# Performance work log

Measured on AMD Instinct MI355X. Metric: run time of the kernel, lower is better.

## Reference

```python
import jax, jax.numpy as jnp
import numpy as np
from jax.scipy.special import gammaln

T_STEPS, N_GRID, NMUL = 730, 10000, 2
NEARZERO = 1e-5
LENF = 15  # unit-hydrograph length used by UH_gamma routing
STAT_NAMES = ["parFC", "parK0", "parK1", "parK2", "parLP", "parPERC", "parUZL",
              "parTT", "parCFMAX", "parCFR", "parCWH", "parC", "parRT", "parAC"]
BOUNDS = {"parBETA": (1.0, 6.0), "parFC": (50.0, 1000.0), "parK0": (0.05, 0.9),
          "parK1": (0.01, 0.5), "parK2": (0.001, 0.2), "parLP": (0.2, 1.0),
          "parPERC": (0.0, 10.0), "parUZL": (0.0, 100.0), "parTT": (-2.5, 2.5),
          "parCFMAX": (0.5, 10.0), "parCFR": (0.0, 0.1), "parCWH": (0.0, 0.2),
          "parBETAET": (0.3, 5.0), "parC": (0.0, 1.0), "parRT": (0.0, 20.0),
          "parAC": (0.0, 2500.0)}
ROUT_A = (0.0, 2.9)
ROUT_B = (0.0, 6.5)


def _scale(p, lo, hi):
    # change_param_range: affine map of [0,1]-normalized params to physical bounds
    return p * (hi - lo) + lo


def setup_inputs() -> dict:
    key = jax.random.key(0)
    ks = jax.random.split(key, 7)
    prcp = jax.random.uniform(ks[0], (T_STEPS, N_GRID)) * 10.0          # mm/day
    tmean = jax.random.uniform(ks[1], (T_STEPS, N_GRID)) * 30.0 - 10.0  # deg C, spans parTT range
    pet = jax.random.uniform(ks[2], (T_STEPS, N_GRID)) * 5.0            # mm/day
    x_phy = jnp.stack([prcp, tmean, pet], axis=-1).astype(jnp.float32)
    ac_all = jax.random.uniform(ks[3], (N_GRID,)) * 2500.0              # drainage area per unit basin
    elev_all = jax.random.uniform(ks[4], (N_GRID,)) * 3000.0            # elevation
    params_dy = jax.random.uniform(ks[5], (T_STEPS, N_GRID, 2 * NMUL))  # dynamic: parBETA, parBETAET
    params_stat = jax.random.uniform(ks[6], (N_GRID, 14 * NMUL + 2))    # 14 static phy + 2 routing
    return {"x_phy": x_phy, "ac_all": ac_all, "elev_all": elev_all,
            "params_dy": params_dy, "params_stat": params_stat}


def _forward(x_phy, ac_all, elev_all, params_dy, params_stat):
    T, G, _ = x_phy.shape
    P, Tair, PET = x_phy[..., 0], x_phy[..., 1], x_phy[..., 2]
    # expand forcing to nmul parameter components
    Pm = jnp.broadcast_to(P[..., None], (T, G, NMUL))
    Tm = jnp.broadcast_to(Tair[..., None], (T, G, NMUL))
    PETm = jnp.broadcast_to(PET[..., None], (T, G, NMUL))
    Ac = jnp.broadcast_to(ac_all[:, None], (G, NMUL))

    # dynamic (per-timestep) params; dy_drop=0.0 -> bernoulli drop mask is all zeros,
    # so the dynamic values are used directly at every step
    dy = params_dy.reshape(T, G, 2, NMUL)
    parBETA = _scale(dy[:, :, 0], *BOUNDS["parBETA"])
    parBETAET = _scale(dy[:, :, 1], *BOUNDS["parBETAET"])

    # static params: [G, 14, NMUL]
    stat = params_stat[:, :14 * NMUL].reshape(G, 14, NMUL)
    sp = {n: _scale(stat[:, i], *BOUNDS[n]) for i, n in enumerate(STAT_NAMES)}
    rout_a = _scale(params_stat[:, 14 * NMUL], *ROUT_A)
    rout_b = _scale(params_stat[:, 14 * NMUL + 1], *ROUT_B)

    def step(carry, xt):
        SNOWPACK, MELTWATER, SM, SUZ, SLZ = carry
        Pt, Tt, PETt, beta, betaet = xt
        rain_mask = (Tt >= sp["parTT"]).astype(Pt.dtype)
        RAIN = Pt * rain_mask
        SNOW = Pt * (1.0 - rain_mask)
        # --- snow bucket ---
        SNOWPACK = SNOWPACK + SNOW
        melt = jnp.maximum(sp["parCFMAX"] * (Tt - sp["parTT"]), 0.0)
        melt = jnp.minimum(melt, SNOWPACK)
        MELTWATER = MELTWATER + melt
        SNOWPACK = SNOWPACK - melt
        refreeze = jnp.maximum(sp["parCFR"] * sp["parCFMAX"] * (sp["parTT"] - Tt), 0.0)
        refreeze = jnp.minimum(refreeze, MELTWATER)
        SNOWPACK = SNOWPACK + refreeze
        MELTWATER = MELTWATER - refreeze
        tosoil = jnp.maximum(MELTWATER - sp["parCWH"] * SNOWPACK, 0.0)
        MELTWATER = MELTWATER - tosoil
        # --- soil bucket ---
        soil_wetness = jnp.clip((SM / sp["parFC"]) ** beta, 0.0, 1.0)
        recharge = (RAIN + tosoil) * soil_wetness
        SM = SM + RAIN + tosoil - recharge
        excess = jnp.maximum(SM - sp["parFC"], 0.0)
        SM = SM - excess
        evapfactor = jnp.clip(SM / (sp["parLP"] * sp["parFC"]), 0.0, 1.0) ** betaet
        ETact = jnp.minimum(SM, PETt * evapfactor)
        SM = jnp.maximum(SM - ETact, NEARZERO)
        # capillary rise from lower groundwater zone (parC)
        capillary = jnp.minimum(SLZ, sp["parC"] * SLZ * (1.0 - jnp.minimum(SM / sp["parFC"], 1.0)))
        SM = jnp.maximum(SM + capillary, NEARZERO)
        SLZ = jnp.maximum(SLZ - capillary, NEARZERO)
        # --- groundwater buckets ---
        SUZ = SUZ + recharge + excess
        PERC = jnp.minimum(SUZ, sp["parPERC"])
        SUZ = SUZ - PERC
        Q0 = sp["parK0"] * jnp.maximum(SUZ - sp["parUZL"], 0.0)
        SUZ = SUZ - Q0
        Q1 = sp["parK1"] * SUZ
        SUZ = SUZ - Q1
        SLZ = SLZ + PERC
        # HBV 2.0 regional groundwater loss (area-dependent via parRT / parAC; reconstructed)
        gw_loss = jnp.minimum(SLZ, sp["parRT"] * jnp.clip(1.0 - Ac / (sp["parAC"] + NEARZERO), 0.0, 1.0))
        SLZ = SLZ - gw_loss
        Q2 = sp["parK2"] * SLZ
        SLZ = SLZ - Q2
        Qt = Q0 + Q1 + Q2
        return (SNOWPACK, MELTWATER, SM, SUZ, SLZ), Qt

    init = tuple(jnp.full((G, NMUL), 1e-3, dtype=x_phy.dtype) for _ in range(5))
    _, Qsimmu = jax.lax.scan(step, init, (Pm, Tm, PETm, parBETA, parBETAET))
    Qsim = Qsimmu.mean(-1)  # [T, G]; muwts=None -> uniform average over nmul components

    # --- gamma unit-hydrograph routing (UH_gamma + causal UH_conv) ---
    a = jnp.maximum(rout_a, 0.0) + 0.1       # [G]
    theta = jnp.maximum(rout_b, 0.0) + 0.5   # [G]
    t = jnp.arange(LENF, dtype=Qsim.dtype) + 0.5  # [LENF]
    w = (jnp.exp(-gammaln(a))[None, :] * theta[None, :] ** (-a[None, :])
         * t[:, None] ** (a[None, :] - 1.0) * jnp.exp(-t[:, None] / theta[None, :]))
    w = w / w.sum(0)  # [LENF, G], normalized UH weights
    # causal grouped conv: flow[t] = sum_k w[k] * Qsim[t-k]
    Qpad = jnp.pad(Qsim, ((LENF - 1, 0), (0, 0)))
    flow = jnp.zeros_like(Qsim)
    for k in range(LENF):  # fixed, small tap count
        flow = flow + w[k][None, :] * Qpad[LENF - 1 - k: LENF - 1 - k + T]
    return flow[..., None]  # [T, G, 1] routed streamflow


def reference(x_phy, ac_all, elev_all, params_dy, params_stat):
    return _forward(x_phy, ac_all, elev_all, params_dy, params_stat)
```

## Files before the change

### kernel.cpp

```cpp
#include <hip/hip_runtime.h>


#define TS 730
#define NG 10000
#define CH 15
#define NCHUNK 49
#define XSTRIDE (NG * 3)
#define DSTRIDE (NG * 4)

#define AS1 __attribute__((address_space(1)))
#define AS3 __attribute__((address_space(3)))
#define WAIT_VMCNT(n) __builtin_amdgcn_s_waitcnt(((n) & 15) | 0x70 | 0xF00 | (((n) >> 4) << 14))
#define WAIT_LGKM0    __builtin_amdgcn_s_waitcnt(0xC07F)

__device__ __forceinline__ void gload16(const float* g, float* l) {
    __builtin_amdgcn_global_load_lds((const AS1 void*)g, (AS3 void*)l, 16, 0, 0);
}
__device__ __forceinline__ float powpos(float x, float b) {
    return __builtin_amdgcn_exp2f(b * __builtin_amdgcn_logf(x));
}
__device__ __forceinline__ float med3(float x, float lo, float hi) {
    return __builtin_amdgcn_fmed3f(x, lo, hi);
}

__global__ __launch_bounds__(64, 1) void hbv_fused(
    const float* __restrict__ x_phy,
    const float* __restrict__ ac_all,
    const float* __restrict__ params_dy,
    const float* __restrict__ params_stat,
    float* __restrict__ out)
{
    __shared__ float xls0[1536], xls1[1536];
    __shared__ float dls0[2048], dls1[2048];

    const int lane = threadIdx.x & 63;
    const int m    = lane >> 5;
    const int cell = lane & 31;
    const int g0   = blockIdx.x * 32;
    const int g    = g0 + cell;
    const int gl   = g < NG ? g : NG - 1;
    const int g0r  = (g0 <= NG - 32) ? g0 : NG - 32;
    const int co   = cell + (g0 - g0r);
    const int cl   = co < 31 ? co : 31;

    const float* ps = params_stat + (size_t)gl * 30;
    const float FC    = ps[0  + m] * 950.f   + 50.f;
    const float K0    = ps[2  + m] * 0.85f   + 0.05f;
    const float K1    = ps[4  + m] * 0.49f   + 0.01f;
    const float K2    = ps[6  + m] * 0.199f  + 0.001f;
    const float LP    = ps[8  + m] * 0.8f    + 0.2f;
    const float PERCp = ps[10 + m] * 10.f;
    const float UZL   = ps[12 + m] * 100.f;
    const float TTp   = ps[14 + m] * 5.f     - 2.5f;
    const float CFMAX = ps[16 + m] * 9.5f    + 0.5f;
    const float CFR   = ps[18 + m] * 0.1f;
    const float CWH   = ps[20 + m] * 0.2f;
    const float Cc    = ps[22 + m];
    const float RT    = ps[24 + m] * 20.f;
    const float ACp   = ps[26 + m] * 2500.f;
    const float ra    = ps[28] * 2.9f;
    const float rb    = ps[29] * 6.5f;

    const float Acv     = ac_all[gl];
    const float invFC   = 1.f / FC;
    const float invLPFC = 1.f / (LP * FC);
    const float CFRC    = CFR * CFMAX;
    const float gwcap   = RT * fminf(fmaxf(1.f - Acv / (ACp + 1e-5f), 0.f), 1.f);

    const float a     = fmaxf(ra, 0.f) + 0.1f;
    const float th    = fmaxf(rb, 0.f) + 0.5f;
    const float am1   = a - 1.f;
    const float nl2e  = 1.44269504f / th;
    float w[CH];
    float wsum = 0.f;
#pragma unroll
    for (int k = 0; k < CH; ++k) {
        const float tk = (float)k + 0.5f;
        const float v  = __builtin_amdgcn_exp2f(am1 * __builtin_amdgcn_logf(tk) - tk * nl2e);
        w[k] = v; wsum += v;
    }
    const float wn = 0.5f / wsum;
#pragma unroll
    for (int k = 0; k < CH; ++k) w[k] *= wn;

    int offx[6], offd[8];
#pragma unroll
    for (int i = 0; i < 6; ++i) {
        int idx = i * 64 + lane;
        idx = idx < 360 ? idx : 359;
        const int row = idx / 24;
        const int col = idx - row * 24;
        offx[i] = row * XSTRIDE + col * 4;
    }
#pragma unroll
    for (int i = 0; i < 8; ++i) {
        int idx = i * 64 + lane;
        idx = idx < 480 ? idx : 479;
        const int row = idx >> 5;
        const int col = idx & 31;
        offd[i] = row * DSTRIDE + col * 4;
    }
    const float* xbase = x_phy     + (size_t)g0r * 3;
    const float* dbase = params_dy + (size_t)g0r * 4;

    auto issue = [&](int cc, float* xl, float* dl) {
        if (cc == NCHUNK - 1) {
#pragma unroll
            for (int i = 0; i < 6; ++i) {
                int idx = i * 64 + lane; idx = idx < 360 ? idx : 359;
                const int row = idx / 24, col = idx - row * 24;
                int t = cc * CH + row; t = t < TS ? t : TS - 1;
                gload16(xbase + (size_t)t * XSTRIDE + col * 4, xl + i * 256);
            }
#pragma unroll
            for (int i = 0; i < 8; ++i) {
                int idx = i * 64 + lane; idx = idx < 480 ? idx : 479;
                const int row = idx >> 5, col = idx & 31;
                int t = cc * CH + row; t = t < TS ? t : TS - 1;
                gload16(dbase + (size_t)t * DSTRIDE + col * 4, dl + i * 256);
            }
        } else {
            const float* xp = xbase + (size_t)cc * CH * XSTRIDE;
            const float* dp = dbase + (size_t)cc * CH * DSTRIDE;
#pragma unroll
            for (int i = 0; i < 6; ++i) gload16(xp + offx[i], xl + i * 256);
#pragma unroll
            for (int i = 0; i < 8; ++i) gload16(dp + offd[i], dl + i * 256);
        }
    };

    float SP = 1e-3f, MW = 1e-3f, SM = 1e-3f, SUZ = 1e-3f, SLZ = 1e-3f;
    float facc[CH];
#pragma unroll
    for (int k = 0; k < CH; ++k) facc[k] = 0.f;

    const bool doStore = (g < NG) && (lane < 32);

    auto chunk = [&](int c, const float* xl, const float* dl) {
        float qts[CH];
        float Pc = xl[cl * 3 + 0], Tc = xl[cl * 3 + 1], Ec = xl[cl * 3 + 2];
        float4 dvc = *(const float4*)&dl[cl * 4];
#pragma unroll
        for (int j = 0; j < CH; ++j) {
            float Pn, Tn, En; float4 dvn;
            if (j < CH - 1) {
                Pn  = xl[(j + 1) * 96 + cl * 3 + 0];
                Tn  = xl[(j + 1) * 96 + cl * 3 + 1];
                En  = xl[(j + 1) * 96 + cl * 3 + 2];
                dvn = *(const float4*)&dl[(j + 1) * 128 + cl * 4];
            }
            const float Pt = Pc, Tt = Tc, PETt = Ec;
            const float beta   = (m ? dvc.y : dvc.x) * 5.f  + 1.f;
            const float betaet = (m ? dvc.w : dvc.z) * 4.7f + 0.3f;

            const float rain = (Tt >= TTp) ? Pt : 0.f;
            SP += Pt - rain;
            const float melt = med3(CFMAX * (Tt - TTp), 0.f, SP);
            MW += melt; SP -= melt;
            const float refr = med3(CFRC * (TTp - Tt), 0.f, MW);
            SP += refr; MW -= refr;
            const float tosoil = fmaxf(MW - CWH * SP, 0.f);
            MW -= tosoil;

            const float sw  = fminf(powpos(SM * invFC, beta), 1.f);
            const float rts = rain + tosoil;
            SM = fmaf(rts, 1.f - sw, SM);
            const float exc = fmaxf(SM - FC, 0.f);
            SM = fminf(SM, FC);
            const float ef = powpos(fminf(SM * invLPFC, 1.f), betaet);
            const float ET = fminf(SM, PETt * ef);
            SM = fmaxf(SM - ET, 1e-5f);
            const float cap = Cc * SLZ * (1.f - fminf(SM * invFC, 1.f));
            SM  = fmaxf(SM + cap, 1e-5f);
            SLZ = fmaxf(SLZ - cap, 1e-5f);

            SUZ += rts * sw + exc;
            const float perc = fminf(SUZ, PERCp);
            SUZ -= perc;
            const float Q0 = K0 * fmaxf(SUZ - UZL, 0.f);
            SUZ -= Q0;
            const float Q1 = K1 * SUZ;
            SUZ -= Q1;
            SLZ += perc;
            SLZ = fmaxf(SLZ - gwcap, 0.f);
            const float Q2 = K2 * SLZ;
            SLZ -= Q2;
            qts[j] = Q0 + Q1 + Q2;

            Pc = Pn; Tc = Tn; Ec = En; dvc = dvn;
        }

        float ofl[CH];
#pragma unroll
        for (int j = 0; j < CH; ++j) {
#pragma unroll
            for (int k = 0; k < CH; ++k)
                facc[(j + k) % CH] = fmaf(w[k], qts[j], facc[(j + k) % CH]);
            ofl[j]  = facc[j];
            facc[j] = 0.f;
        }

        float prt[CH];
#pragma unroll
        for (int jj = 0; jj < CH; ++jj) prt[jj] = __shfl_xor(ofl[jj], 32);
        if (doStore) {
            float* op = out + (size_t)c * CH * NG + g;
            const int tb = c * CH;
#pragma unroll
            for (int jj = 0; jj < CH; ++jj)
                if (tb + jj < TS) op[(size_t)jj * NG] = ofl[jj] + prt[jj];
        }
    };

    issue(0, xls0, dls0);
    issue(1, xls1, dls1);

    WAIT_VMCNT(14);
    chunk(0, xls0, dls0);
    WAIT_LGKM0;
    issue(2, xls0, dls0);
    WAIT_VMCNT(29);
    chunk(1, xls1, dls1);
    WAIT_LGKM0;
    issue(3, xls1, dls1);

    for (int cp = 1; cp < 24; ++cp) {
        const int c0 = 2 * cp;
        WAIT_VMCNT(29);
        chunk(c0, xls0, dls0);
        WAIT_LGKM0;
        issue(c0 + 2, xls0, dls0);
        WAIT_VMCNT(29);
        chunk(c0 + 1, xls1, dls1);
        WAIT_LGKM0;
        if (cp < 23) issue(c0 + 3, xls1, dls1);
    }
    WAIT_VMCNT(15);
    chunk(48, xls0, dls0);
}

extern "C" void kernel_launch(void* const* d_in, const int* in_sizes, int n_in,
                              void* d_out, int out_size, void* d_ws, size_t ws_size,
                              hipStream_t stream) {
    const float* x_phy = (const float*)d_in[0];
    const float* ac    = (const float*)d_in[1];
    const float* pdy   = (const float*)d_in[3];
    const float* pst   = (const float*)d_in[4];
    float* out = (float*)d_out;

    const int grid = (NG + 31) / 32;
    hbv_fused<<<grid, 64, 0, stream>>>(x_phy, ac, pdy, pst, out);
}
```

Baseline: 320.5 us.

## Split scan and routing into producer/consumer warps with LDS handoff

Each block now runs two wavefronts. Wave 0 runs the serial HBV state recurrence and writes per-step discharge into double-buffered LDS. Wave 1 issues the global-to-LDS forcing loads, does the gamma unit-hydrograph convolution and stores the output. The goal is to take the load issue, convolution FMAs and global stores off the latency-critical recurrence and run them concurrently, using block barriers for handoff. There are also small algebra tweaks: the refreeze coefficient is negated, C*SLZ is precomputed, and the ET min is dropped. This adds barrier synchronization per chunk and doubles the threads per block, and the ET/cap rewrites could slightly change numerics.

```diff
diff --git a/kernel.cpp b/kernel.cpp
--- a/kernel.cpp
+++ b/kernel.cpp
@@ -12,6 +12,8 @@
 #define AS3 __attribute__((address_space(3)))
 #define WAIT_VMCNT(n) __builtin_amdgcn_s_waitcnt(((n) & 15) | 0x70 | 0xF00 | (((n) >> 4) << 14))
 #define WAIT_LGKM0    __builtin_amdgcn_s_waitcnt(0xC07F)
+#define SBAR          __builtin_amdgcn_s_barrier
+#define SCHED_FENCE() __builtin_amdgcn_sched_barrier(0)
 
 __device__ __forceinline__ void gload16(const float* g, float* l) {
     __builtin_amdgcn_global_load_lds((const AS1 void*)g, (AS3 void*)l, 16, 0, 0);
@@ -23,7 +25,7 @@
     return __builtin_amdgcn_fmed3f(x, lo, hi);
 }
 
-__global__ __launch_bounds__(64, 1) void hbv_fused(
+__global__ __launch_bounds__(128, 1) void hbv_fused(
     const float* __restrict__ x_phy,
     const float* __restrict__ ac_all,
     const float* __restrict__ params_dy,
@@ -32,8 +34,11 @@
 {
     __shared__ float xls0[1536], xls1[1536];
     __shared__ float dls0[2048], dls1[2048];
-
-    const int lane = threadIdx.x & 63;
+    __shared__ float qb0[960], qb1[960];
+
+    const int tid  = threadIdx.x;
+    const int wid  = tid >> 6;
+    const int lane = tid & 63;
     const int m    = lane >> 5;
     const int cell = lane & 31;
     const int g0   = blockIdx.x * 32;
@@ -64,7 +69,7 @@
     const float Acv     = ac_all[gl];
     const float invFC   = 1.f / FC;
     const float invLPFC = 1.f / (LP * FC);
-    const float CFRC    = CFR * CFMAX;
+    const float nCFRC   = -(CFR * CFMAX);
     const float gwcap   = RT * fminf(fmaxf(1.f - Acv / (ACp + 1e-5f), 0.f), 1.f);
 
     const float a     = fmaxf(ra, 0.f) + 0.1f;
@@ -129,114 +134,116 @@
         }
     };
 
-    float SP = 1e-3f, MW = 1e-3f, SM = 1e-3f, SUZ = 1e-3f, SLZ = 1e-3f;
-    float facc[CH];
-#pragma unroll
-    for (int k = 0; k < CH; ++k) facc[k] = 0.f;
-
-    const bool doStore = (g < NG) && (lane < 32);
-
-    auto chunk = [&](int c, const float* xl, const float* dl) {
-        float qts[CH];
-        float Pc = xl[cl * 3 + 0], Tc = xl[cl * 3 + 1], Ec = xl[cl * 3 + 2];
-        float4 dvc = *(const float4*)&dl[cl * 4];
-#pragma unroll
-        for (int j = 0; j < CH; ++j) {
-            float Pn, Tn, En; float4 dvn;
-            if (j < CH - 1) {
-                Pn  = xl[(j + 1) * 96 + cl * 3 + 0];
-                Tn  = xl[(j + 1) * 96 + cl * 3 + 1];
-                En  = xl[(j + 1) * 96 + cl * 3 + 2];
-                dvn = *(const float4*)&dl[(j + 1) * 128 + cl * 4];
-            }
-            const float Pt = Pc, Tt = Tc, PETt = Ec;
-            const float beta   = (m ? dvc.y : dvc.x) * 5.f  + 1.f;
-            const float betaet = (m ? dvc.w : dvc.z) * 4.7f + 0.3f;
-
-            const float rain = (Tt >= TTp) ? Pt : 0.f;
-            SP += Pt - rain;
-            const float melt = med3(CFMAX * (Tt - TTp), 0.f, SP);
-            MW += melt; SP -= melt;
-            const float refr = med3(CFRC * (TTp - Tt), 0.f, MW);
-            SP += refr; MW -= refr;
-            const float tosoil = fmaxf(MW - CWH * SP, 0.f);
-            MW -= tosoil;
-
-            const float sw  = fminf(powpos(SM * invFC, beta), 1.f);
-            const float rts = rain + tosoil;
-            SM = fmaf(rts, 1.f - sw, SM);
-            const float exc = fmaxf(SM - FC, 0.f);
-            SM = fminf(SM, FC);
-            const float ef = powpos(fminf(SM * invLPFC, 1.f), betaet);
-            const float ET = fminf(SM, PETt * ef);
-            SM = fmaxf(SM - ET, 1e-5f);
-            const float cap = Cc * SLZ * (1.f - fminf(SM * invFC, 1.f));
-            SM  = fmaxf(SM + cap, 1e-5f);
-            SLZ = fmaxf(SLZ - cap, 1e-5f);
-
-            SUZ += rts * sw + exc;
-            const float perc = fminf(SUZ, PERCp);
-            SUZ -= perc;
-            const float Q0 = K0 * fmaxf(SUZ - UZL, 0.f);
-            SUZ -= Q0;
-            const float Q1 = K1 * SUZ;
-            SUZ -= Q1;
-            SLZ += perc;
-            SLZ = fmaxf(SLZ - gwcap, 0.f);
-            const float Q2 = K2 * SLZ;
-            SLZ -= Q2;
-            qts[j] = Q0 + Q1 + Q2;
-
-            Pc = Pn; Tc = Tn; Ec = En; dvc = dvn;
+    if (wid == 0) {
+        float SP = 1e-3f, MW = 1e-3f, SM = 1e-3f, SUZ = 1e-3f, SLZ = 1e-3f;
+        float CcSLZ = Cc * 1e-3f;
+
+        auto scan = [&](const float* xl, const float* dl, float* qb) {
+            float Pc = xl[cl * 3 + 0], Tc = xl[cl * 3 + 1], Ec = xl[cl * 3 + 2];
+            float4 dvc = *(const float4*)&dl[cl * 4];
+#pragma unroll
+            for (int j = 0; j < CH; ++j) {
+                float Pn, Tn, En; float4 dvn;
+                if (j < CH - 1) {
+                    Pn  = xl[(j + 1) * 96 + cl * 3 + 0];
+                    Tn  = xl[(j + 1) * 96 + cl * 3 + 1];
+                    En  = xl[(j + 1) * 96 + cl * 3 + 2];
+                    dvn = *(const float4*)&dl[(j + 1) * 128 + cl * 4];
+                }
+                const float beta   = fmaf(m ? dvc.y : dvc.x, 5.f, 1.f);
+                const float betaet = fmaf(m ? dvc.w : dvc.z, 4.7f, 0.3f);
+
+                const float t1   = Tc - TTp;
+                const float snow = (t1 < 0.f) ? Pc : 0.f;
+                const float rain = Pc - snow;
+                SP += snow;
+                const float melt = med3(CFMAX * t1, 0.f, SP);
+                MW += melt; SP -= melt;
+                const float refr = med3(nCFRC * t1, 0.f, MW);
+                SP += refr; MW -= refr;
+                const float tosoil = fmaxf(MW - CWH * SP, 0.f);
+                MW -= tosoil;
+
+                const float sw  = fminf(powpos(SM * invFC, beta), 1.f);
+                const float rts = rain + tosoil;
+                SM = fmaf(rts, 1.f - sw, SM);
+                const float exc = fmaxf(SM - FC, 0.f);
+                SM = fminf(SM, FC);
+                const float ef = powpos(fminf(SM * invLPFC, 1.f), betaet);
+                SM = fmaxf(SM - Ec * ef, 1e-5f);
+                const float cap = CcSLZ * fmaxf(1.f - SM * invFC, 0.f);
+                SM  = fmaxf(SM + cap, 1e-5f);
+                SLZ = fmaxf(SLZ - cap, 1e-5f);
+
+                SUZ = SUZ + rts * sw + exc;
+                const float perc = fminf(SUZ, PERCp);
+                SUZ -= perc;
+                const float Q0 = K0 * fmaxf(SUZ - UZL, 0.f);
+                SUZ -= Q0;
+                const float Q1 = K1 * SUZ;
+                SUZ -= Q1;
+                SLZ += perc;
+                SLZ = fmaxf(SLZ - gwcap, 0.f);
+                const float Q2 = K2 * SLZ;
+                SLZ -= Q2;
+                CcSLZ = Cc * SLZ;
+                qb[(j << 6) + lane] = Q0 + Q1 + Q2;
+
+                Pc = Pn; Tc = Tn; Ec = En; dvc = dvn;
+            }
+        };
+
+        SBAR();
+        scan(xls0, dls0, qb0);
+        WAIT_LGKM0; SCHED_FENCE();
+        for (int cp = 0; cp < 24; ++cp) {
+            SBAR();
+            scan(xls1, dls1, qb1);
+            WAIT_LGKM0; SCHED_FENCE();
+            SBAR();
+            scan(xls0, dls0, qb0);
+            WAIT_LGKM0; SCHED_FENCE();
         }
-
-        float ofl[CH];
-#pragma unroll
-        for (int j = 0; j < CH; ++j) {
-#pragma unroll
-            for (int k = 0; k < CH; ++k)
-                facc[(j + k) % CH] = fmaf(w[k], qts[j], facc[(j + k) % CH]);
-            ofl[j]  = facc[j];
-            facc[j] = 0.f;
-        }
-
-        float prt[CH];
-#pragma unroll
-        for (int jj = 0; jj < CH; ++jj) prt[jj] = __shfl_xor(ofl[jj], 32);
-        if (doStore) {
+        SBAR();
+    } else {
+        float facc[CH];
+#pragma unroll
+        for (int k = 0; k < CH; ++k) facc[k] = 0.f;
+        const bool doStore = (g < NG) && (lane < 32);
+        const int  l32 = lane & 31;
+
+        auto conv = [&](int c, const float* qb) {
             float* op = out + (size_t)c * CH * NG + g;
             const int tb = c * CH;
 #pragma unroll
-            for (int jj = 0; jj < CH; ++jj)
-                if (tb + jj < TS) op[(size_t)jj * NG] = ofl[jj] + prt[jj];
+            for (int j = 0; j < CH; ++j) {
+                const float qm = qb[(j << 6) + l32] + qb[(j << 6) + 32 + l32];
+#pragma unroll
+                for (int k = 0; k < CH; ++k)
+                    facc[(j + k) % CH] = fmaf(w[k], qm, facc[(j + k) % CH]);
+                if (doStore && (tb + j < TS)) op[(size_t)j * NG] = facc[j];
+                facc[j] = 0.f;
+            }
+        };
+
+        issue(0, xls0, dls0);
+        WAIT_VMCNT(0); SCHED_FENCE();
+        SBAR();
+        issue(1, xls1, dls1);
+        WAIT_VMCNT(0); SCHED_FENCE();
+        SBAR();
+        for (int cp = 0; cp < 24; ++cp) {
+            issue(2 * cp + 2, xls0, dls0);
+            conv(2 * cp, qb0);
+            WAIT_VMCNT(15); SCHED_FENCE();
+            SBAR();
+            if (cp < 23) issue(2 * cp + 3, xls1, dls1);
+            conv(2 * cp + 1, qb1);
+            WAIT_VMCNT(15); SCHED_FENCE();
+            SBAR();
         }
-    };
-
-    issue(0, xls0, dls0);
-    issue(1, xls1, dls1);
-
-    WAIT_VMCNT(14);
-    chunk(0, xls0, dls0);
-    WAIT_LGKM0;
-    issue(2, xls0, dls0);
-    WAIT_VMCNT(29);
-    chunk(1, xls1, dls1);
-    WAIT_LGKM0;
-    issue(3, xls1, dls1);
-
-    for (int cp = 1; cp < 24; ++cp) {
-        const int c0 = 2 * cp;
-        WAIT_VMCNT(29);
-        chunk(c0, xls0, dls0);
-        WAIT_LGKM0;
-        issue(c0 + 2, xls0, dls0);
-        WAIT_VMCNT(29);
-        chunk(c0 + 1, xls1, dls1);
-        WAIT_LGKM0;
-        if (cp < 23) issue(c0 + 3, xls1, dls1);
-    }
-    WAIT_VMCNT(15);
-    chunk(48, xls0, dls0);
+        conv(48, qb0);
+    }
 }
 
 extern "C" void kernel_launch(void* const* d_in, const int* in_sizes, int n_in,
@@ -249,5 +256,5 @@
     float* out = (float*)d_out;
 
     const int grid = (NG + 31) / 32;
-    hbv_fused<<<grid, 64, 0, stream>>>(x_phy, ac, pdy, pst, out);
-}
+    hbv_fused<<<grid, 128, 0, stream>>>(x_phy, ac, pdy, pst, out);
+}
```

Result: faster. 276.0 us (-13.9%).
